# Kernel optimization log

Measured on AMD Instinct MI355X. Metric: run time of the kernel, lower is better.

The kernel has to match this reference:

```python
import jax, jax.numpy as jnp
import numpy as np
from jax import lax

FIR_TAPS = np.array([1.0, 3.0, 3.0, 1.0], dtype=np.float32)
FACTOR = 2
GAIN = 1.0


def _fir_kernel(C):
    # _setup_kernel: outer product, normalize to sum 1; upsample scales by gain*factor**2
    k = np.outer(FIR_TAPS, FIR_TAPS)
    k = k / k.sum() * (GAIN * FACTOR ** 2)  # 4x4 kernel, sum == 4
    k = jnp.asarray(k, jnp.float32)
    return jnp.tile(k[None, None], (C, 1, 1, 1))  # [C,1,4,4] depthwise


def setup_inputs() -> dict:
    key = jax.random.key(0)
    k1, k2, k3 = jax.random.split(key, 3)
    x = jax.random.normal(k1, (16, 256, 64, 64), jnp.float32)
    W = jax.random.normal(k2, (256, 256, 3, 3), jnp.float32) * 0.02
    b = jax.random.normal(k3, (256,), jnp.float32) * 0.02
    return {"x": x, "W": W, "b": b}


def reference(x, W, b):
    B, C, H, Wd = x.shape
    kern = _fir_kernel(C)
    # upfirdn2d upsample: zero-insert by 2 (lhs_dilation), pad0=2 / pad1=1(+up-1=2),
    # depthwise FIR correlation -> [B, C, 2H, 2W]
    p0, p1 = 2, 2  # pad1 = p//2 + (factor-1) trailing zeros folded into padding
    h = lax.conv_general_dilated(
        x, kern, window_strides=(1, 1), padding=((p0, p1), (p0, p1)),
        lhs_dilation=(FACTOR, FACTOR),
        dimension_numbers=("NCHW", "OIHW", "NCHW"), feature_group_count=C)
    # 3x3 conv, padding=1, stride=1 -> [B, out_ch, 2H, 2W]
    y = lax.conv_general_dilated(
        h, W, window_strides=(1, 1), padding=((1, 1), (1, 1)),
        dimension_numbers=("NCHW", "OIHW", "NCHW"))
    return y + b[None, :, None, None]
```

## Files before the change

kernel.cpp:

```cpp
#include <hip/hip_runtime.h>
#include <hip/hip_bf16.h>
#include <stdint.h>

typedef __attribute__((ext_vector_type(8))) short bf16x8;
typedef __attribute__((ext_vector_type(4))) float f32x4;

#define PH 130
#define NT 36

__device__ __forceinline__ short f2bf(float f) {
  uint32_t u = __builtin_bit_cast(uint32_t, f);
  u = (u + 0x7FFFu + ((u >> 16) & 1u)) >> 16;
  return (short)u;
}

__device__ __forceinline__ void gload16(const void* g, void* l) {
  __builtin_amdgcn_global_load_lds(
      (const __attribute__((address_space(1))) void*)g,
      (__attribute__((address_space(3))) void*)l, 16, 0, 0);
}

__global__ void wpack(const float* __restrict__ W, short* __restrict__ A) {
  int tid = blockIdx.x * 256 + threadIdx.x;
  if (tid >= 256 * 2304) return;
  int co = tid / 2304;
  int r  = tid - co * 2304;
  int tap = r >> 8, ci = r & 255;
  A[tid] = f2bf(W[((size_t)(co * 256 + ci)) * 9 + tap]);
}

__global__ void fir_up(const float* __restrict__ x, short* __restrict__ hT) {
  const int bp = blockIdx.x;
  const int b = bp / PH, pp = bp - b * PH;
  const int ci0 = blockIdx.y << 6;
  const int t = threadIdx.x;
  short* outrow = hT + ((size_t)(b * PH + pp) * PH) * 256 + ci0;

  if (pp == 0 || pp == PH - 1) {
    for (int idx = t; idx < PH * 64; idx += 256) {
      int qp = idx >> 6, c = idx & 63;
      outrow[(size_t)qp * 256 + c] = 0;
    }
    return;
  }
  const int p = pp - 1;
  int i0, i1; float wr0, wr1;
  if (!(p & 1)) { i0 = (p >> 1) - 1; i1 = p >> 1;     wr0 = 0.25f; wr1 = 0.75f; }
  else          { i0 = p >> 1;       i1 = (p >> 1)+1; wr0 = 0.75f; wr1 = 0.25f; }

  __shared__ float X[2][64][65];
#pragma unroll
  for (int r = 0; r < 2; ++r) {
    int ir = r ? i1 : i0;
    bool ok = (ir >= 0 && ir < 64);
#pragma unroll
    for (int it = 0; it < 4; ++it) {
      int idx = it * 256 + t;
      int ci = idx >> 4, jq = idx & 15;
      f32x4 v = {0.f, 0.f, 0.f, 0.f};
      if (ok)
        v = *(const f32x4*)&x[((size_t)(b * 256 + ci0 + ci) * 64 + ir) * 64 + jq * 4];
      X[r][jq * 4 + 0][ci] = v[0];
      X[r][jq * 4 + 1][ci] = v[1];
      X[r][jq * 4 + 2][ci] = v[2];
      X[r][jq * 4 + 3][ci] = v[3];
    }
  }
  __syncthreads();

  const int c = t & 63;
  for (int qp = (t >> 6); qp < PH; qp += 4) {
    float val = 0.f;
    if (qp >= 1 && qp <= 128) {
      int q = qp - 1;
      int j0, j1; float wc0, wc1;
      if (!(q & 1)) { j0 = (q >> 1) - 1; j1 = q >> 1; wc0 = 0.25f; wc1 = 0.75f; }
      else          { j0 = q >> 1;       j1 = j0 + 1; wc0 = 0.75f; wc1 = 0.25f; }
      float v00 = (j0 >= 0) ? X[0][j0][c] : 0.f;
      float v10 = (j0 >= 0) ? X[1][j0][c] : 0.f;
      float v01 = (j1 < 64) ? X[0][j1][c] : 0.f;
      float v11 = (j1 < 64) ? X[1][j1][c] : 0.f;
      val = wr0 * (wc0 * v00 + wc1 * v01) + wr1 * (wc0 * v10 + wc1 * v11);
    }
    outrow[(size_t)qp * 256 + c] = f2bf(val);
  }
}

__global__ __launch_bounds__(512) void conv3x3_gemm(
    const short* __restrict__ hT, const short* __restrict__ Wp,
    const float* __restrict__ bias, float* __restrict__ y) {
  __shared__ short ldsA[2][16384];
  __shared__ short ldsB[2][16384];
  const int tid = threadIdx.x;
  const int lane = tid & 63, w = tid >> 6;
  const int wm = w >> 2, wn = w & 3;

  const int bid = blockIdx.x;
  const int tile = (bid & 7) * 128 + (bid >> 3);
  const int b = tile >> 6, p0 = (tile & 63) * 2;

  const short* srcA[4];
  const short* srcB[4];
#pragma unroll
  for (int h = 0; h < 2; ++h)
#pragma unroll
    for (int i = 0; i < 2; ++i) {
      int o = h * 16384 + i * 8192 + w * 1024 + lane * 16;
      int L = o ^ (((o >> 7) & 7) << 4);
      int row = L >> 7, kk = (L & 127) >> 1;
      int pr = row >> 7, q = row & 127;
      srcA[h * 2 + i] = hT + ((size_t)((b * PH + p0 + pr) * PH + q)) * 256 + kk;
      srcB[h * 2 + i] = Wp + (size_t)row * 2304 + kk;
    }

  auto offA = [&](int t) {
    int tap = t >> 2, ci0 = (t & 3) << 6;
    int dm = (tap >= 6) ? 2 : (tap >= 3) ? 1 : 0;
    int dn = tap - 3 * dm;
    return (dm * PH + dn) * 256 + ci0;
  };
  auto offB = [&](int t) { return (t >> 2) * 256 + ((t & 3) << 6); };

  auto stageA = [&](int t) {
    int o = offA(t);
    short* dst = &ldsA[t & 1][0];
#pragma unroll
    for (int j = 0; j < 4; ++j)
      gload16(srcA[j] + o, dst + (j >> 1) * 8192 + (j & 1) * 4096 + w * 512);
  };
  auto stageB = [&](int t) {
    int o = offB(t);
    short* dst = &ldsB[t & 1][0];
#pragma unroll
    for (int j = 0; j < 4; ++j)
      gload16(srcB[j] + o, dst + (j >> 1) * 8192 + (j & 1) * 4096 + w * 512);
  };

  int aP[2], bP[2];
#pragma unroll
  for (int ks = 0; ks < 2; ++ks) {
    int La = (wm * 128 + (lane & 15)) * 128 + (lane >> 4) * 16 + ks * 64;
    aP[ks] = La ^ ((lane & 7) << 4);
    int Lb = (wn * 64 + (lane & 15)) * 128 + (lane >> 4) * 16 + ks * 64;
    bP[ks] = Lb ^ ((lane & 7) << 4);
  }

  f32x4 acc[8][4];
#pragma unroll
  for (int m = 0; m < 8; ++m)
#pragma unroll
    for (int n = 0; n < 4; ++n) acc[m][n] = (f32x4){0.f, 0.f, 0.f, 0.f};

  stageB(0); stageA(0); stageB(1);
  asm volatile("s_waitcnt vmcnt(4)" ::: "memory");
  __builtin_amdgcn_s_barrier();

  for (int t = 0; t < NT; ++t) {
    const char* LA = (const char*)&ldsA[t & 1][0];
    const char* LB = (const char*)&ldsB[t & 1][0];

    bf16x8 a0[4], a1[4], b0[4], b1[4];
#pragma unroll
    for (int m = 0; m < 4; ++m) {
      a0[m] = *(const bf16x8*)(LA + aP[0] + m * 2048);
      a1[m] = *(const bf16x8*)(LA + aP[1] + m * 2048);
    }
#pragma unroll
    for (int n = 0; n < 4; ++n) {
      b0[n] = *(const bf16x8*)(LB + bP[0] + n * 2048);
      b1[n] = *(const bf16x8*)(LB + bP[1] + n * 2048);
    }
    if (t + 1 < NT) stageA(t + 1);
    __builtin_amdgcn_s_barrier();
    asm volatile("s_waitcnt lgkmcnt(0)" ::: "memory");
    __builtin_amdgcn_sched_barrier(0);
    __builtin_amdgcn_s_setprio(1);
#pragma unroll
    for (int m = 0; m < 4; ++m)
#pragma unroll
      for (int n = 0; n < 4; ++n) {
        acc[m][n] = __builtin_amdgcn_mfma_f32_16x16x32_bf16(a0[m], b0[n], acc[m][n], 0, 0, 0);
        acc[m][n] = __builtin_amdgcn_mfma_f32_16x16x32_bf16(a1[m], b1[n], acc[m][n], 0, 0, 0);
      }
    __builtin_amdgcn_s_setprio(0);
    __builtin_amdgcn_s_barrier();

    bf16x8 c0[4], c1[4];
#pragma unroll
    for (int m = 0; m < 4; ++m) {
      c0[m] = *(const bf16x8*)(LA + aP[0] + (m + 4) * 2048);
      c1[m] = *(const bf16x8*)(LA + aP[1] + (m + 4) * 2048);
    }
    if (t + 2 < NT) stageB(t + 2);
    __builtin_amdgcn_s_barrier();
    asm volatile("s_waitcnt lgkmcnt(0)" ::: "memory");
    __builtin_amdgcn_sched_barrier(0);
    __builtin_amdgcn_s_setprio(1);
#pragma unroll
    for (int m = 0; m < 4; ++m)
#pragma unroll
      for (int n = 0; n < 4; ++n) {
        acc[m + 4][n] = __builtin_amdgcn_mfma_f32_16x16x32_bf16(c0[m], b0[n], acc[m + 4][n], 0, 0, 0);
        acc[m + 4][n] = __builtin_amdgcn_mfma_f32_16x16x32_bf16(c1[m], b1[n], acc[m + 4][n], 0, 0, 0);
      }
    __builtin_amdgcn_s_setprio(0);
    if (t == NT - 2)      asm volatile("s_waitcnt vmcnt(0)" ::: "memory");
    else if (t < NT - 2)  asm volatile("s_waitcnt vmcnt(4)" ::: "memory");
    if (t < NT - 1) __builtin_amdgcn_s_barrier();
  }

#pragma unroll
  for (int n = 0; n < 4; ++n) {
    int co = wn * 64 + n * 16 + (lane & 15);
    float bv = bias[co];
    float* yp = y + (((size_t)(b * 256 + co)) * 128 + (p0 + wm)) * 128;
#pragma unroll
    for (int m = 0; m < 8; ++m) {
      int q0 = m * 16 + ((lane >> 4) << 2);
      f32x4 v = acc[m][n];
      v[0] += bv; v[1] += bv; v[2] += bv; v[3] += bv;
      *(f32x4*)(yp + q0) = v;
    }
  }
}

extern "C" void kernel_launch(void* const* d_in, const int* in_sizes, int n_in,
                              void* d_out, int out_size, void* d_ws, size_t ws_size,
                              hipStream_t stream) {
  const float* x    = (const float*)d_in[0];
  const float* W    = (const float*)d_in[1];
  const float* bias = (const float*)d_in[2];
  float* y = (float*)d_out;

  const size_t hT_bytes = (size_t)16 * PH * PH * 256 * 2;
  const size_t A_bytes  = (size_t)256 * 2304 * 2;
  if (ws_size < hT_bytes + A_bytes) return;

  short* hT = (short*)d_ws;
  short* Wp = (short*)((char*)d_ws + hT_bytes);

  wpack<<<(256 * 2304 + 255) / 256, 256, 0, stream>>>(W, Wp);
  dim3 g1(16 * PH, 4);
  fir_up<<<g1, 256, 0, stream>>>(x, hT);
  conv3x3_gemm<<<1024, 512, 0, stream>>>(hT, Wp, bias, y);
}
```

Measured before the change: 429.5 us.

## Shrink GEMM tiles with triple-buffered A, restructure FIR upsample to pair rows

The conv GEMM tile shrinks from 256x256 to 128x128, so 4096 blocks run instead of 1024, with occupancy hint 4. A now uses a three-stage LDS buffer and each K-step needs a single barrier. The FIR kernel computes two output rows per block from a vertically pre-filtered LDS tile and writes bf16 pairs as 32-bit stores. The goal is better occupancy and less sync overhead, at the cost of lower data reuse per block and more global traffic for A and B.

```diff
diff --git a/kernel.cpp b/kernel.cpp
--- a/kernel.cpp
+++ b/kernel.cpp
@@ -12,6 +12,10 @@
   uint32_t u = __builtin_bit_cast(uint32_t, f);
   u = (u + 0x7FFFu + ((u >> 16) & 1u)) >> 16;
   return (short)u;
+}
+
+__device__ __forceinline__ uint32_t pack2bf(float lo, float hi) {
+  return ((uint32_t)(uint16_t)f2bf(hi) << 16) | (uint16_t)f2bf(lo);
 }
 
 __device__ __forceinline__ void gload16(const void* g, void* l) {
@@ -30,88 +34,87 @@
 }
 
 __global__ void fir_up(const float* __restrict__ x, short* __restrict__ hT) {
-  const int bp = blockIdx.x;
-  const int b = bp / PH, pp = bp - b * PH;
+  const int bt = blockIdx.x;
+  const int b = bt / 65, t = bt - b * 65;
   const int ci0 = blockIdx.y << 6;
-  const int t = threadIdx.x;
-  short* outrow = hT + ((size_t)(b * PH + pp) * PH) * 256 + ci0;
-
-  if (pp == 0 || pp == PH - 1) {
-    for (int idx = t; idx < PH * 64; idx += 256) {
-      int qp = idx >> 6, c = idx & 63;
-      outrow[(size_t)qp * 256 + c] = 0;
+  const int tid = threadIdx.x;
+
+  if (t == 64) {
+    short* r0 = hT + ((size_t)(b * PH + 0) * PH) * 256 + ci0;
+    short* r1 = hT + ((size_t)(b * PH + 129) * PH) * 256 + ci0;
+    for (int idx = tid; idx < PH * 32; idx += 256) {
+      int qp = idx >> 5, c2 = (idx & 31) * 2;
+      *(uint32_t*)&r0[(size_t)qp * 256 + c2] = 0u;
+      *(uint32_t*)&r1[(size_t)qp * 256 + c2] = 0u;
     }
     return;
   }
-  const int p = pp - 1;
-  int i0, i1; float wr0, wr1;
-  if (!(p & 1)) { i0 = (p >> 1) - 1; i1 = p >> 1;     wr0 = 0.25f; wr1 = 0.75f; }
-  else          { i0 = p >> 1;       i1 = (p >> 1)+1; wr0 = 0.75f; wr1 = 0.25f; }
-
-  __shared__ float X[2][64][65];
+
+  __shared__ float F[2][64][65];
+#pragma unroll
+  for (int it = 0; it < 4; ++it) {
+    int idx = it * 256 + tid;
+    int ci = idx >> 4, jq = idx & 15;
+    const float* base = &x[((size_t)(b * 256 + ci0 + ci) * 64) * 64 + jq * 4];
+    f32x4 vm = {0.f, 0.f, 0.f, 0.f}, vp = {0.f, 0.f, 0.f, 0.f};
+    f32x4 v0 = *(const f32x4*)(base + (size_t)t * 64);
+    if (t >= 1)  vm = *(const f32x4*)(base + (size_t)(t - 1) * 64);
+    if (t <= 62) vp = *(const f32x4*)(base + (size_t)(t + 1) * 64);
+#pragma unroll
+    for (int e = 0; e < 4; ++e) {
+      F[0][jq * 4 + e][ci] = 0.25f * vm[e] + 0.75f * v0[e];
+      F[1][jq * 4 + e][ci] = 0.75f * v0[e] + 0.25f * vp[e];
+    }
+  }
+  __syncthreads();
+
+  const int c2 = (tid & 31) * 2;
+  const int qg = tid >> 5;
 #pragma unroll
   for (int r = 0; r < 2; ++r) {
-    int ir = r ? i1 : i0;
-    bool ok = (ir >= 0 && ir < 64);
-#pragma unroll
-    for (int it = 0; it < 4; ++it) {
-      int idx = it * 256 + t;
-      int ci = idx >> 4, jq = idx & 15;
-      f32x4 v = {0.f, 0.f, 0.f, 0.f};
-      if (ok)
-        v = *(const f32x4*)&x[((size_t)(b * 256 + ci0 + ci) * 64 + ir) * 64 + jq * 4];
-      X[r][jq * 4 + 0][ci] = v[0];
-      X[r][jq * 4 + 1][ci] = v[1];
-      X[r][jq * 4 + 2][ci] = v[2];
-      X[r][jq * 4 + 3][ci] = v[3];
-    }
-  }
-  __syncthreads();
-
-  const int c = t & 63;
-  for (int qp = (t >> 6); qp < PH; qp += 4) {
-    float val = 0.f;
-    if (qp >= 1 && qp <= 128) {
-      int q = qp - 1;
-      int j0, j1; float wc0, wc1;
-      if (!(q & 1)) { j0 = (q >> 1) - 1; j1 = q >> 1; wc0 = 0.25f; wc1 = 0.75f; }
-      else          { j0 = q >> 1;       j1 = j0 + 1; wc0 = 0.75f; wc1 = 0.25f; }
-      float v00 = (j0 >= 0) ? X[0][j0][c] : 0.f;
-      float v10 = (j0 >= 0) ? X[1][j0][c] : 0.f;
-      float v01 = (j1 < 64) ? X[0][j1][c] : 0.f;
-      float v11 = (j1 < 64) ? X[1][j1][c] : 0.f;
-      val = wr0 * (wc0 * v00 + wc1 * v01) + wr1 * (wc0 * v10 + wc1 * v11);
-    }
-    outrow[(size_t)qp * 256 + c] = f2bf(val);
-  }
-}
-
-__global__ __launch_bounds__(512) void conv3x3_gemm(
+    short* outrow = hT + ((size_t)(b * PH + (2 * t + 1 + r)) * PH) * 256 + ci0;
+    for (int qp = qg; qp < PH; qp += 8) {
+      uint32_t out = 0u;
+      if (qp >= 1 && qp <= 128) {
+        int q = qp - 1;
+        int par = q & 1;
+        int jb = (q >> 1) - 1 + par;
+        float wc0 = par ? 0.75f : 0.25f;
+        float wc1 = par ? 0.25f : 0.75f;
+        float v00 = 0.f, v01 = 0.f, v10 = 0.f, v11 = 0.f;
+        if (jb >= 0)     { v00 = F[r][jb][c2];     v01 = F[r][jb][c2 + 1]; }
+        if (jb + 1 < 64) { v10 = F[r][jb + 1][c2]; v11 = F[r][jb + 1][c2 + 1]; }
+        out = pack2bf(wc0 * v00 + wc1 * v10, wc0 * v01 + wc1 * v11);
+      }
+      *(uint32_t*)&outrow[(size_t)qp * 256 + c2] = out;
+    }
+  }
+}
+
+__global__ __launch_bounds__(512, 4) void conv3x3_gemm(
     const short* __restrict__ hT, const short* __restrict__ Wp,
     const float* __restrict__ bias, float* __restrict__ y) {
-  __shared__ short ldsA[2][16384];
-  __shared__ short ldsB[2][16384];
+  __shared__ short ldsA[3][8192];
+  __shared__ short ldsB[2][8192];
   const int tid = threadIdx.x;
   const int lane = tid & 63, w = tid >> 6;
   const int wm = w >> 2, wn = w & 3;
 
   const int bid = blockIdx.x;
-  const int tile = (bid & 7) * 128 + (bid >> 3);
-  const int b = tile >> 6, p0 = (tile & 63) * 2;
-
-  const short* srcA[4];
-  const short* srcB[4];
-#pragma unroll
-  for (int h = 0; h < 2; ++h)
-#pragma unroll
-    for (int i = 0; i < 2; ++i) {
-      int o = h * 16384 + i * 8192 + w * 1024 + lane * 16;
-      int L = o ^ (((o >> 7) & 7) << 4);
-      int row = L >> 7, kk = (L & 127) >> 1;
-      int pr = row >> 7, q = row & 127;
-      srcA[h * 2 + i] = hT + ((size_t)((b * PH + p0 + pr) * PH + q)) * 256 + kk;
-      srcB[h * 2 + i] = Wp + (size_t)row * 2304 + kk;
-    }
+  const int tau = (bid & 7) * 512 + (bid >> 3);
+  const int mt = tau >> 1, nh = tau & 1;
+  const int b = mt >> 7, p = mt & 127;
+
+  const short* srcA[2];
+  const short* srcB[2];
+#pragma unroll
+  for (int i = 0; i < 2; ++i) {
+    int o = i * 8192 + w * 1024 + lane * 16;
+    int L = o ^ (((o >> 7) & 7) << 4);
+    int row = L >> 7, kk = (L & 127) >> 1;
+    srcA[i] = hT + ((size_t)((b * PH + p) * PH + row)) * 256 + kk;
+    srcB[i] = Wp + (size_t)(nh * 128 + row) * 2304 + kk;
+  }
 
   auto offA = [&](int t) {
     int tap = t >> 2, ci0 = (t & 3) << 6;
@@ -123,103 +126,78 @@
 
   auto stageA = [&](int t) {
     int o = offA(t);
-    short* dst = &ldsA[t & 1][0];
-#pragma unroll
-    for (int j = 0; j < 4; ++j)
-      gload16(srcA[j] + o, dst + (j >> 1) * 8192 + (j & 1) * 4096 + w * 512);
+    short* dst = &ldsA[t % 3][0];
+#pragma unroll
+    for (int i = 0; i < 2; ++i)
+      gload16(srcA[i] + o, dst + i * 4096 + w * 512);
   };
   auto stageB = [&](int t) {
     int o = offB(t);
     short* dst = &ldsB[t & 1][0];
 #pragma unroll
-    for (int j = 0; j < 4; ++j)
-      gload16(srcB[j] + o, dst + (j >> 1) * 8192 + (j & 1) * 4096 + w * 512);
+    for (int i = 0; i < 2; ++i)
+      gload16(srcB[i] + o, dst + i * 4096 + w * 512);
   };
 
   int aP[2], bP[2];
 #pragma unroll
   for (int ks = 0; ks < 2; ++ks) {
-    int La = (wm * 128 + (lane & 15)) * 128 + (lane >> 4) * 16 + ks * 64;
+    int La = (wm * 64 + (lane & 15)) * 128 + (lane >> 4) * 16 + ks * 64;
     aP[ks] = La ^ ((lane & 7) << 4);
-    int Lb = (wn * 64 + (lane & 15)) * 128 + (lane >> 4) * 16 + ks * 64;
+    int Lb = (wn * 32 + (lane & 15)) * 128 + (lane >> 4) * 16 + ks * 64;
     bP[ks] = Lb ^ ((lane & 7) << 4);
   }
 
-  f32x4 acc[8][4];
-#pragma unroll
-  for (int m = 0; m < 8; ++m)
-#pragma unroll
-    for (int n = 0; n < 4; ++n) acc[m][n] = (f32x4){0.f, 0.f, 0.f, 0.f};
-
-  stageB(0); stageA(0); stageB(1);
-  asm volatile("s_waitcnt vmcnt(4)" ::: "memory");
+  f32x4 acc[4][2];
+#pragma unroll
+  for (int m = 0; m < 4; ++m)
+#pragma unroll
+    for (int n = 0; n < 2; ++n) acc[m][n] = (f32x4){0.f, 0.f, 0.f, 0.f};
+
+  stageA(0); stageB(0); stageA(1);
+  asm volatile("s_waitcnt vmcnt(2)" ::: "memory");
   __builtin_amdgcn_s_barrier();
 
   for (int t = 0; t < NT; ++t) {
-    const char* LA = (const char*)&ldsA[t & 1][0];
+    const char* LA = (const char*)&ldsA[t % 3][0];
     const char* LB = (const char*)&ldsB[t & 1][0];
 
-    bf16x8 a0[4], a1[4], b0[4], b1[4];
-#pragma unroll
-    for (int m = 0; m < 4; ++m) {
-      a0[m] = *(const bf16x8*)(LA + aP[0] + m * 2048);
-      a1[m] = *(const bf16x8*)(LA + aP[1] + m * 2048);
-    }
-#pragma unroll
-    for (int n = 0; n < 4; ++n) {
-      b0[n] = *(const bf16x8*)(LB + bP[0] + n * 2048);
-      b1[n] = *(const bf16x8*)(LB + bP[1] + n * 2048);
-    }
-    if (t + 1 < NT) stageA(t + 1);
-    __builtin_amdgcn_s_barrier();
+    bf16x8 a_[2][4], b_[2][2];
+#pragma unroll
+    for (int ks = 0; ks < 2; ++ks) {
+#pragma unroll
+      for (int m = 0; m < 4; ++m) a_[ks][m] = *(const bf16x8*)(LA + aP[ks] + m * 2048);
+#pragma unroll
+      for (int n = 0; n < 2; ++n) b_[ks][n] = *(const bf16x8*)(LB + bP[ks] + n * 2048);
+    }
+    if (t + 1 < NT) stageB(t + 1);
+    if (t + 2 < NT) stageA(t + 2);
     asm volatile("s_waitcnt lgkmcnt(0)" ::: "memory");
-    __builtin_amdgcn_sched_barrier(0);
     __builtin_amdgcn_s_setprio(1);
 #pragma unroll
     for (int m = 0; m < 4; ++m)
 #pragma unroll
-      for (int n = 0; n < 4; ++n) {
-        acc[m][n] = __builtin_amdgcn_mfma_f32_16x16x32_bf16(a0[m], b0[n], acc[m][n], 0, 0, 0);
-        acc[m][n] = __builtin_amdgcn_mfma_f32_16x16x32_bf16(a1[m], b1[n], acc[m][n], 0, 0, 0);
+      for (int n = 0; n < 2; ++n) {
+        acc[m][n] = __builtin_amdgcn_mfma_f32_16x16x32_bf16(a_[0][m], b_[0][n], acc[m][n], 0, 0, 0);
+        acc[m][n] = __builtin_amdgcn_mfma_f32_16x16x32_bf16(a_[1][m], b_[1][n], acc[m][n], 0, 0, 0);
       }
     __builtin_amdgcn_s_setprio(0);
+    if (t < NT - 2)       asm volatile("s_waitcnt vmcnt(2)" ::: "memory");
+    else if (t == NT - 2) asm volatile("s_waitcnt vmcnt(0)" ::: "memory");
     __builtin_amdgcn_s_barrier();
-
-    bf16x8 c0[4], c1[4];
+  }
+
+#pragma unroll
+  for (int n = 0; n < 2; ++n) {
+    int co = nh * 128 + wn * 32 + n * 16 + (lane & 15);
+    float bv = bias[co];
+    float* yp = y + (((size_t)(b * 256 + co)) * 128 + p) * 128;
 #pragma unroll
     for (int m = 0; m < 4; ++m) {
-      c0[m] = *(const bf16x8*)(LA + aP[0] + (m + 4) * 2048);
-      c1[m] = *(const bf16x8*)(LA + aP[1] + (m + 4) * 2048);
-    }
-    if (t + 2 < NT) stageB(t + 2);
-    __builtin_amdgcn_s_barrier();
-    asm volatile("s_waitcnt lgkmcnt(0)" ::: "memory");
-    __builtin_amdgcn_sched_barrier(0);
-    __builtin_amdgcn_s_setprio(1);
-#pragma unroll
-    for (int m = 0; m < 4; ++m)
-#pragma unroll
-      for (int n = 0; n < 4; ++n) {
-        acc[m + 4][n] = __builtin_amdgcn_mfma_f32_16x16x32_bf16(c0[m], b0[n], acc[m + 4][n], 0, 0, 0);
-        acc[m + 4][n] = __builtin_amdgcn_mfma_f32_16x16x32_bf16(c1[m], b1[n], acc[m + 4][n], 0, 0, 0);
-      }
-    __builtin_amdgcn_s_setprio(0);
-    if (t == NT - 2)      asm volatile("s_waitcnt vmcnt(0)" ::: "memory");
-    else if (t < NT - 2)  asm volatile("s_waitcnt vmcnt(4)" ::: "memory");
-    if (t < NT - 1) __builtin_amdgcn_s_barrier();
-  }
-
-#pragma unroll
-  for (int n = 0; n < 4; ++n) {
-    int co = wn * 64 + n * 16 + (lane & 15);
-    float bv = bias[co];
-    float* yp = y + (((size_t)(b * 256 + co)) * 128 + (p0 + wm)) * 128;
-#pragma unroll
-    for (int m = 0; m < 8; ++m) {
-      int q0 = m * 16 + ((lane >> 4) << 2);
-      f32x4 v = acc[m][n];
-      v[0] += bv; v[1] += bv; v[2] += bv; v[3] += bv;
-      *(f32x4*)(yp + q0) = v;
+      int q0 = wm * 64 + m * 16 + ((lane >> 4) << 2);
+      f32x4 vv = acc[m][n];
+      vv[0] += bv; vv[1] += bv; vv[2] += bv; vv[3] += bv;
+      *(f32x4*)(yp + q0) = vv;
     }
   }
 }
@@ -240,7 +218,7 @@
   short* Wp = (short*)((char*)d_ws + hT_bytes);
 
   wpack<<<(256 * 2304 + 255) / 256, 256, 0, stream>>>(W, Wp);
-  dim3 g1(16 * PH, 4);
+  dim3 g1(16 * 65, 4);
   fir_up<<<g1, 256, 0, stream>>>(x, hT);
-  conv3x3_gemm<<<1024, 512, 0, stream>>>(hT, Wp, bias, y);
-}
+  conv3x3_gemm<<<4096, 512, 0, stream>>>(hT, Wp, bias, y);
+}
```

Result: faster. 375.7 us, median of 2 (-12.5%).
